# Performance work log

Hardware: AMD Instinct MI355X
Metric: run time of the kernel (lower is better)

The kernel has to match this reference:

```python
import jax, jax.numpy as jnp
import numpy as np

LN_EPS = 1e-5

def _layer_norm(x):
    mu = jnp.mean(x, axis=-1, keepdims=True)
    var = jnp.var(x, axis=-1, keepdims=True)
    return (x - mu) / jnp.sqrt(var + LN_EPS)


def setup_inputs() -> dict:
    key = jax.random.key(0)
    ks = jax.random.split(key, 3)
    B, C, H, W = 8, 384, 48, 48
    x = jax.random.normal(ks[0], (B, C, H, W), dtype=jnp.float32)
    # torch Linear default init ~ U(-1/sqrt(fan_in), 1/sqrt(fan_in)); scaled normal is fine for a reference
    W1 = jax.random.normal(ks[1], (3 * C, C), dtype=jnp.float32) / np.sqrt(C)
    b1 = jnp.zeros((3 * C,), dtype=jnp.float32)
    W2 = jax.random.normal(ks[2], (C, C), dtype=jnp.float32) / np.sqrt(C)
    b2 = jnp.zeros((C,), dtype=jnp.float32)
    return {"x": x, "W1": W1, "b1": b1, "W2": W2, "b2": b2}


def reference(x, W1, b1, W2, b2):
    num_heads = 6
    B, C, H, W = x.shape
    N = H * W
    d = C // num_heads
    # [B,C,H,W] -> [B,N,C]
    t = x.reshape(B, C, N).transpose(0, 2, 1)
    t_norm = _layer_norm(t)
    qkv = t_norm @ W1.T + b1                      # [B,N,3C]
    q, k, v = jnp.split(qkv, 3, axis=-1)
    q = q.reshape(B, N, num_heads, d).transpose(0, 2, 1, 3)  # [B,h,N,d]
    k = k.reshape(B, N, num_heads, d).transpose(0, 2, 1, 3)
    v = v.reshape(B, N, num_heads, d).transpose(0, 2, 1, 3)
    att = jnp.einsum('bhnd,bhmd->bhnm', q, k) / jnp.sqrt(jnp.float32(d))
    att = jax.nn.softmax(att, axis=-1)            # dropout_prob = 0.0 -> identity
    o = jnp.einsum('bhnm,bhmd->bhnd', att, v)     # [B,h,N,d]
    o = o.transpose(0, 2, 1, 3).reshape(B, N, C)
    o = o @ W2.T + b2
    out = (o + t_norm).transpose(0, 2, 1).reshape(B, C, H, W)
    return out
```

## Files before the change

### kernel.cpp

```cpp
#include <hip/hip_runtime.h>
#include <cstdint>

#define DEVI __device__ __forceinline__

typedef unsigned short u16;
typedef __attribute__((ext_vector_type(4))) u16 u16x4;
typedef __attribute__((ext_vector_type(2))) unsigned int u32x2;
typedef __attribute__((ext_vector_type(2))) float f32x2;
typedef __attribute__((ext_vector_type(4))) float f32x4;
typedef __attribute__((ext_vector_type(8))) float f32x8;
typedef __attribute__((ext_vector_type(16))) float f32x16;
typedef __attribute__((ext_vector_type(8))) __bf16 bf16x8;

constexpr int kB = 8, kC = 384, kN = 2304, kNH = 6, kD = 64;
constexpr int kM = kB * kN;
constexpr int k3C = 3 * kC;
constexpr int kNT = kN / 64;
constexpr int kKS = kC / 32;

DEVI float bf2f(u16 u) {
  union { unsigned int u; float f; } v; v.u = ((unsigned int)u) << 16; return v.f;
}
DEVI u16 f2bf(float f) {
  union { float f; unsigned int u; } v; v.f = f;
  return (u16)((v.u + 0x7fffu + ((v.u >> 16) & 1u)) >> 16);
}
DEVI void gload16(const void* g, void* l) {
  __builtin_amdgcn_global_load_lds(
      (__attribute__((address_space(1))) void*)const_cast<void*>(g),
      (__attribute__((address_space(3))) void*)l, 16, 0, 0);
}
DEVI bf16x8 ldg8(const u16* p) { return *reinterpret_cast<const bf16x8*>(p); }

DEVI float fexp2(float x) {
#if __has_builtin(__builtin_amdgcn_exp2f)
  return __builtin_amdgcn_exp2f(x);
#else
  return exp2f(x);
#endif
}

DEVI unsigned cvtpk(float lo, float hi) {
  unsigned r;
  asm("v_cvt_pk_bf16_f32 %0, %1, %2" : "=v"(r) : "v"(lo), "v"(hi));
  return r;
}
DEVI void plswap(unsigned& a, unsigned& b) {
#if __has_builtin(__builtin_amdgcn_permlane32_swap)
  auto rr = __builtin_amdgcn_permlane32_swap(a, b, false, false);
  a = rr[0]; b = rr[1];
#else
  unsigned ax = __shfl_xor(a, 32, 64), bx = __shfl_xor(b, 32, 64);
  int hi = (threadIdx.x & 63) >> 5;
  unsigned r0 = hi ? bx : a;
  unsigned r1 = hi ? b : ax;
  a = r0; b = r1;
#endif
}

DEVI bf16x8 ldsw(const u16* base, int row, int cb) {
  return *reinterpret_cast<const bf16x8*>(
      (const char*)base + row * 128 + (cb ^ ((row & 7) << 4)));
}

__global__ __launch_bounds__(256) void ln_kernel(const float* __restrict__ x,
                                                 u16* __restrict__ tn) {
  const int b = blockIdx.x & 7;
  const int n0 = (blockIdx.x >> 3) * 64;
  const int t = threadIdx.x;
  const int tni = t & 63, tc = t >> 6;
  const float* xb = x + (size_t)b * kC * kN;

  float sum = 0.f, ssq = 0.f;
  for (int c = tc; c < kC; c += 4) {
    float v = xb[(size_t)c * kN + n0 + tni];
    sum += v; ssq += v * v;
  }
  __shared__ float red[8][64];
  red[tc][tni] = sum; red[tc + 4][tni] = ssq;
  __syncthreads();
  __shared__ float s_mu[64], s_rs[64];
  if (t < 64) {
    float s = red[0][t] + red[1][t] + red[2][t] + red[3][t];
    float q = red[4][t] + red[5][t] + red[6][t] + red[7][t];
    float mu = s * (1.f / kC);
    float var = q * (1.f / kC) - mu * mu;
    s_mu[t] = mu; s_rs[t] = rsqrtf(var + 1e-5f);
  }
  __syncthreads();
  __shared__ float tile[64][65];
  for (int c0 = 0; c0 < kC; c0 += 64) {
#pragma unroll
    for (int kk = 0; kk < 16; ++kk) {
      int cl = tc * 16 + kk;
      tile[tni][cl] = xb[(size_t)(c0 + cl) * kN + n0 + tni];
    }
    __syncthreads();
#pragma unroll
    for (int kk = 0; kk < 16; ++kk) {
      int nl = tc * 16 + kk;
      float v = (tile[nl][tni] - s_mu[nl]) * s_rs[nl];
      tn[((size_t)b * kN + n0 + nl) * kC + c0 + tni] = f2bf(v);
    }
    __syncthreads();
  }
}

__global__ __launch_bounds__(256) void cast_w(const float* __restrict__ W1, const float* __restrict__ W2,
                                              u16* __restrict__ w1b, u16* __restrict__ w2b) {
  int i = blockIdx.x * 256 + threadIdx.x;
  if (i < k3C * kC) w1b[i] = f2bf(W1[i]);
  if (i < kC * kC)  w2b[i] = f2bf(W2[i]);
}

DEVI int swzg(int r, int sl) { return (sl ^ ((r >> 1) & 3)) * 8; }

#define GSTAGE(dstLds, gbase, kt)                                        \
  {                                                                      \
    _Pragma("unroll")                                                    \
    for (int c = 0; c < 2; ++c) {                                        \
      int i = c * 256 + t;                                               \
      int r = i >> 2, sl = i & 3;                                        \
      gload16((gbase) + (size_t)r * kC + (kt) + swzg(r, sl),             \
              (dstLds) + (c * 256 + (t & 192)) * 8);                     \
    }                                                                    \
  }

DEVI void gemm_core(const u16* __restrict__ A, const u16* __restrict__ Bm,
                    f32x4 acc[4][4], u16* lA, u16* lB) {
  const int t = threadIdx.x;
  const int lane = t & 63;
  const int w = t >> 6, wr = w >> 1, wc = w & 1;
  const int lr = lane & 15, lg = lane >> 4;

  GSTAGE(lA, A, 0)
  GSTAGE(lB, Bm, 0)

  int cur = 0;
#pragma unroll 3
  for (int s = 0; s < kKS; ++s) {
    const u16* cA = lA + cur * 4096;
    const u16* cB = lB + cur * 4096;
    const int nxt = (cur == 2) ? 0 : cur + 1;
    if (s + 1 < kKS) {
      GSTAGE(lA + nxt * 4096, A, (s + 1) * 32)
      GSTAGE(lB + nxt * 4096, Bm, (s + 1) * 32)
      asm volatile("s_waitcnt vmcnt(4)" ::: "memory");
    } else {
      asm volatile("s_waitcnt vmcnt(0)" ::: "memory");
    }
    __builtin_amdgcn_s_barrier();
    __builtin_amdgcn_sched_barrier(0);

    bf16x8 af[4], bfr[4];
#pragma unroll
    for (int f = 0; f < 4; ++f) {
      int row = wr * 64 + f * 16 + lr;
      af[f] = ldg8(&cA[row * 32 + swzg(row, lg)]);
    }
#pragma unroll
    for (int f = 0; f < 4; ++f) {
      int row = wc * 64 + f * 16 + lr;
      bfr[f] = ldg8(&cB[row * 32 + swzg(row, lg)]);
    }
    __builtin_amdgcn_s_setprio(1);
#pragma unroll
    for (int fm = 0; fm < 4; ++fm)
#pragma unroll
      for (int fn = 0; fn < 4; ++fn)
        acc[fm][fn] = __builtin_amdgcn_mfma_f32_16x16x32_bf16(af[fm], bfr[fn], acc[fm][fn], 0, 0, 0);
    __builtin_amdgcn_s_setprio(0);
    cur = nxt;
  }
}

__global__ __launch_bounds__(256) void qkv_kernel(const u16* __restrict__ tn, const u16* __restrict__ w1b,
                                                  const float* __restrict__ b1,
                                                  u16* __restrict__ q, u16* __restrict__ kbuf,
                                                  u16* __restrict__ vTout) {
  __shared__ u16 shmem[6 * 4096];
  const int wg = blockIdx.x;
  const int xcd = wg & 7, idx = wg >> 3;
  const int m0 = (xcd * 18 + idx / 9) * 128;
  const int o0 = (idx % 9) * 128;
  f32x4 acc[4][4] = {};
  gemm_core(tn + (size_t)m0 * kC, w1b + (size_t)o0 * kC, acc, shmem, shmem + 3 * 4096);

  const int t = threadIdx.x, lane = t & 63, w = t >> 6;
  const int wr = w >> 1, wc = w & 1, lr = lane & 15, lg = lane >> 4;
  const float kQScale = 0.125f * 1.44269504088896f;
  const int bb = m0 / kN;
  const int nb0 = m0 % kN;
  const int ot = o0 >> 7;

  if (ot >= 6) {
#pragma unroll
    for (int fn = 0; fn < 4; ++fn) {
      int ol = o0 - 2 * kC + wc * 64 + fn * 16 + lr;
      float bias = b1[2 * kC + ol];
      int h = ol >> 6, dd = ol & 63;
#pragma unroll
      for (int fm = 0; fm < 4; ++fm) {
        int n4 = nb0 + wr * 64 + fm * 16 + lg * 4;
        u16x4 pk;
#pragma unroll
        for (int r = 0; r < 4; ++r) pk[r] = f2bf(acc[fm][fn][r] + bias);
        *reinterpret_cast<u16x4*>(&vTout[(((size_t)bb * kNH + h) * kD + dd) * kN + n4]) = pk;
      }
    }
  } else {
    __syncthreads();
    const float scale = (ot < 3) ? kQScale : 1.0f;
#pragma unroll
    for (int fn = 0; fn < 4; ++fn) {
      int col = wc * 64 + fn * 16 + lr;
      float bias = b1[o0 + col];
#pragma unroll
      for (int fm = 0; fm < 4; ++fm)
#pragma unroll
        for (int r = 0; r < 4; ++r) {
          int row = wr * 64 + fm * 16 + lg * 4 + r;
          shmem[row * 132 + col] = f2bf((acc[fm][fn][r] + bias) * scale);
        }
    }
    __syncthreads();
    u16* outp = (ot < 3) ? q : kbuf;
    const int h0 = (o0 - (ot < 3 ? 0 : kC)) >> 6;
#pragma unroll
    for (int it = 0; it < 8; ++it) {
      int ci = it * 256 + t;
      int row = ci >> 4, ck = ci & 15;
      int c = ck * 8;
      int h = h0 + (c >> 6), dd = c & 63;
      *reinterpret_cast<bf16x8*>(&outp[(((size_t)bb * kNH + h) * kN + nb0 + row) * kD + dd]) =
          *reinterpret_cast<const bf16x8*>(&shmem[row * 132 + c]);
    }
  }
}

#define PV_STEP(SV, OFF, KS)                                                          \
  {                                                                                   \
    unsigned a0 = cvtpk(SV[OFF + 0], SV[OFF + 1]);                                    \
    unsigned a1 = cvtpk(SV[OFF + 2], SV[OFF + 3]);                                    \
    unsigned a2 = cvtpk(SV[OFF + 4], SV[OFF + 5]);                                    \
    unsigned a3 = cvtpk(SV[OFF + 6], SV[OFF + 7]);                                    \
    plswap(a0, a2); plswap(a1, a3);                                                   \
    union { unsigned wds[4]; bf16x8 v; } pu;                                          \
    pu.wds[0] = a0; pu.wds[1] = a1; pu.wds[2] = a2; pu.wds[3] = a3;                   \
    bf16x8 vf0 = ldsw(vL, ql, (KS) * 32 + hi * 16);                                   \
    bf16x8 vf1 = ldsw(vL, 32 + ql, (KS) * 32 + hi * 16);                              \
    o0 = __builtin_amdgcn_mfma_f32_32x32x16_bf16(vf0, pu.v, o0, 0, 0, 0);             \
    o1 = __builtin_amdgcn_mfma_f32_32x32x16_bf16(vf1, pu.v, o1, 0, 0, 0);             \
    o2 = __builtin_amdgcn_mfma_f32_32x32x16_bf16(onesf, pu.v, o2, 0, 0, 0);           \
  }

#define STAGE(dstLds, gbase, gstride)                                                 \
  {                                                                                   \
    int r_ = t >> 3;                                                                  \
    int cb_ = ((t & 7) * 16) ^ ((r_ & 7) << 4);                                       \
    gload16((gbase) + (size_t)r_ * (gstride) + cb_,                                   \
            (dstLds) + (t & 448) * 8);                                                \
  }

__global__ __launch_bounds__(512) void attn_kernel(const u16* __restrict__ qg, const u16* __restrict__ kg,
                                                   const u16* __restrict__ vT, u16* __restrict__ obuf) {
  const int wg = blockIdx.x;
  const int xcd = wg & 7, idx = wg >> 3;
  const int bh = xcd * 6 + idx / 9;
  const int qt = idx % 9;
  const int b = bh / kNH, h = bh % kNH;
  const int t = threadIdx.x, lane = t & 63, w = t >> 6;
  const int q0w = qt * 256 + w * 32;
  const int ql = lane & 31;
  const int hi = lane >> 5;
  const u16* qb  = qg + (size_t)bh * kN * kD;
  const char* kbB = (const char*)(kg + (size_t)bh * kN * kD);
  const char* vbT = (const char*)(vT + (size_t)bh * kD * kN);

  __shared__ u16 kLds[3 * 4096];
  __shared__ u16 vLds[3 * 4096];

  bf16x8 qf[4];
#pragma unroll
  for (int ds = 0; ds < 4; ++ds)
    qf[ds] = ldg8(&qb[(size_t)(q0w + ql) * kD + ds * 16 + hi * 8]);

  bf16x8 onesf;
#pragma unroll
  for (int j = 0; j < 8; ++j) onesf[j] = (__bf16)1.0f;

  f32x16 o0 = {}, o1 = {}, o2 = {};

  STAGE(kLds, kbB, 128)
  STAGE(vLds, vbT, kN * 2)

  int cur = 0;
  for (int ti = 0; ti < kNT; ++ti) {
    const u16* kL = kLds + cur * 4096;
    const u16* vL = vLds + cur * 4096;
    const int nxt = (cur == 2) ? 0 : cur + 1;
    if (ti + 1 < kNT) {
      const char* kNext = kbB + (size_t)(ti + 1) * 64 * 128;
      const char* vNext = vbT + (size_t)(ti + 1) * 128;
      STAGE(kLds + nxt * 4096, kNext, 128)
      STAGE(vLds + nxt * 4096, vNext, kN * 2)
      asm volatile("s_waitcnt vmcnt(2)" ::: "memory");
    } else {
      asm volatile("s_waitcnt vmcnt(0)" ::: "memory");
    }
    __builtin_amdgcn_s_barrier();
    __builtin_amdgcn_sched_barrier(0);

    f32x16 s0 = {}, s1 = {};
#pragma unroll
    for (int ds = 0; ds < 4; ++ds) {
      bf16x8 kf0 = ldsw(kL, ql, ds * 32 + hi * 16);
      bf16x8 kf1 = ldsw(kL, 32 + ql, ds * 32 + hi * 16);
      s0 = __builtin_amdgcn_mfma_f32_32x32x16_bf16(kf0, qf[ds], s0, 0, 0, 0);
      s1 = __builtin_amdgcn_mfma_f32_32x32x16_bf16(kf1, qf[ds], s1, 0, 0, 0);
    }

#pragma unroll
    for (int r = 0; r < 16; ++r) {
      s0[r] = fexp2(s0[r]);
      s1[r] = fexp2(s1[r]);
    }

    PV_STEP(s0, 0, 0)
    PV_STEP(s0, 8, 1)
    PV_STEP(s1, 0, 2)
    PV_STEP(s1, 8, 3)

    cur = nxt;
  }

  const float inv = 1.f / o2[0];
  {
    const size_t row = ((size_t)b * kN + q0w + ql) * kC + h * 64;
#pragma unroll
    for (int g = 0; g < 4; ++g) {
      u32x2 pk;
      pk.x = cvtpk(o0[g * 4 + 0] * inv, o0[g * 4 + 1] * inv);
      pk.y = cvtpk(o0[g * 4 + 2] * inv, o0[g * 4 + 3] * inv);
      *reinterpret_cast<u32x2*>(&obuf[row + g * 8 + 4 * hi]) = pk;
    }
#pragma unroll
    for (int g = 0; g < 4; ++g) {
      u32x2 pk;
      pk.x = cvtpk(o1[g * 4 + 0] * inv, o1[g * 4 + 1] * inv);
      pk.y = cvtpk(o1[g * 4 + 2] * inv, o1[g * 4 + 3] * inv);
      *reinterpret_cast<u32x2*>(&obuf[row + 32 + g * 8 + 4 * hi]) = pk;
    }
  }
}

__global__ __launch_bounds__(256) void proj_kernel(const u16* __restrict__ obuf, const u16* __restrict__ w2b,
                                                   const float* __restrict__ b2, const u16* __restrict__ tn,
                                                   float* __restrict__ out) {
  __shared__ u16 lAs[3 * 4096], lBs[3 * 4096];
  const int wg = blockIdx.x;
  const int xcd = wg & 7, idx = wg >> 3;
  const int bn = xcd * 18 + idx / 3;
  const int b = bn / 18;
  const int n0 = (bn % 18) * 128;
  const int c0 = (idx % 3) * 128;
  f32x4 acc[4][4] = {};
  gemm_core(w2b + (size_t)c0 * kC, obuf + ((size_t)b * kN + n0) * kC, acc, lAs, lBs);

  const int t = threadIdx.x, lane = t & 63, w = t >> 6;
  const int wr = w >> 1, wc = w & 1, lr = lane & 15, lg = lane >> 4;
#pragma unroll
  for (int fm = 0; fm < 4; ++fm)
#pragma unroll
    for (int fn = 0; fn < 4; ++fn) {
      int n = n0 + wc * 64 + fn * 16 + lr;
#pragma unroll
      for (int r = 0; r < 4; ++r) {
        int c = c0 + wr * 64 + fm * 16 + lg * 4 + r;
        float val = acc[fm][fn][r] + b2[c] + bf2f(tn[((size_t)b * kN + n) * kC + c]);
        out[((size_t)b * kC + c) * kN + n] = val;
      }
    }
}

extern "C" void kernel_launch(void* const* d_in, const int* in_sizes, int n_in,
                              void* d_out, int out_size, void* d_ws, size_t ws_size,
                              hipStream_t stream) {
  const float* x  = (const float*)d_in[0];
  const float* W1 = (const float*)d_in[1];
  const float* b1 = (const float*)d_in[2];
  const float* W2 = (const float*)d_in[3];
  const float* b2 = (const float*)d_in[4];
  float* out = (float*)d_out;

  const size_t nBNC = (size_t)kM * kC;
  u16* tn  = (u16*)d_ws;
  u16* qb  = tn  + nBNC;
  u16* kb  = qb  + nBNC;
  u16* vb  = kb  + nBNC;
  u16* vT  = vb  + nBNC;
  u16* w1b = vT  + nBNC;
  u16* w2b = w1b + (size_t)k3C * kC;
  u16* obuf = vb;

  ln_kernel<<<dim3(kB * (kN / 64)), dim3(256), 0, stream>>>(x, tn);
  cast_w<<<dim3((k3C * kC + 255) / 256), dim3(256), 0, stream>>>(W1, W2, w1b, w2b);
  qkv_kernel<<<dim3(kM / 128 * (k3C / 128)), dim3(256), 0, stream>>>(tn, w1b, b1, qb, kb, vT);
  attn_kernel<<<dim3((kN / 256) * kB * kNH), dim3(512), 0, stream>>>(qb, kb, vT, obuf);
  proj_kernel<<<dim3((kN / 128) * (kC / 128) * kB), dim3(256), 0, stream>>>(obuf, w2b, b2, tn, out);
}
```

Before: 168.7 us.

## Fuse weight cast into LN kernel, widen QKV GEMM tile, deepen attention prefetch

New measurement: 165.5 us. No clear change (-1.9%).

```diff
diff --git a/kernel.cpp b/kernel.cpp
--- a/kernel.cpp
+++ b/kernel.cpp
@@ -17,6 +17,8 @@
 constexpr int k3C = 3 * kC;
 constexpr int kNT = kN / 64;
 constexpr int kKS = kC / 32;
+constexpr int kW1E = k3C * kC;
+constexpr int kW2E = kC * kC;
 
 DEVI float bf2f(u16 u) {
   union { unsigned int u; float f; } v; v.u = ((unsigned int)u) << 16; return v.f;
@@ -63,8 +65,31 @@
       (const char*)base + row * 128 + (cb ^ ((row & 7) << 4)));
 }
 
-__global__ __launch_bounds__(256) void ln_kernel(const float* __restrict__ x,
-                                                 u16* __restrict__ tn) {
+__global__ __launch_bounds__(256) void ln_cast_kernel(const float* __restrict__ x,
+                                                      u16* __restrict__ tn,
+                                                      const float* __restrict__ W1,
+                                                      const float* __restrict__ W2,
+                                                      u16* __restrict__ w1b,
+                                                      u16* __restrict__ w2b) {
+  if (blockIdx.x >= 288) {
+    const int gid = (blockIdx.x - 288) * 256 + threadIdx.x;
+    const int i4 = gid * 4;
+    if (i4 < kW1E) {
+      f32x4 v = *reinterpret_cast<const f32x4*>(&W1[i4]);
+      u16x4 o;
+#pragma unroll
+      for (int r = 0; r < 4; ++r) o[r] = f2bf(v[r]);
+      *reinterpret_cast<u16x4*>(&w1b[i4]) = o;
+    } else if (i4 < kW1E + kW2E) {
+      const int j = i4 - kW1E;
+      f32x4 v = *reinterpret_cast<const f32x4*>(&W2[j]);
+      u16x4 o;
+#pragma unroll
+      for (int r = 0; r < 4; ++r) o[r] = f2bf(v[r]);
+      *reinterpret_cast<u16x4*>(&w2b[j]) = o;
+    }
+    return;
+  }
   const int b = blockIdx.x & 7;
   const int n0 = (blockIdx.x >> 3) * 64;
   const int t = threadIdx.x;
@@ -104,13 +129,6 @@
     }
     __syncthreads();
   }
-}
-
-__global__ __launch_bounds__(256) void cast_w(const float* __restrict__ W1, const float* __restrict__ W2,
-                                              u16* __restrict__ w1b, u16* __restrict__ w2b) {
-  int i = blockIdx.x * 256 + threadIdx.x;
-  if (i < k3C * kC) w1b[i] = f2bf(W1[i]);
-  if (i < kC * kC)  w2b[i] = f2bf(W2[i]);
 }
 
 DEVI int swzg(int r, int sl) { return (sl ^ ((r >> 1) & 3)) * 8; }
@@ -174,23 +192,88 @@
   }
 }
 
-__global__ __launch_bounds__(256) void qkv_kernel(const u16* __restrict__ tn, const u16* __restrict__ w1b,
+#define GSTAGE2A(dstLds, gbase, kt)                                      \
+  {                                                                      \
+    _Pragma("unroll")                                                    \
+    for (int c = 0; c < 2; ++c) {                                        \
+      int i = c * 512 + t;                                               \
+      int r = i >> 2, sl = i & 3;                                        \
+      gload16((gbase) + (size_t)r * kC + (kt) + swzg(r, sl),             \
+              (dstLds) + (c * 512 + (t & 448)) * 8);                     \
+    }                                                                    \
+  }
+#define GSTAGE2B(dstLds, gbase, kt)                                      \
+  {                                                                      \
+    int r = t >> 2, sl = t & 3;                                          \
+    gload16((gbase) + (size_t)r * kC + (kt) + swzg(r, sl),               \
+            (dstLds) + (t & 448) * 8);                                   \
+  }
+
+DEVI void gemm_core256(const u16* __restrict__ A, const u16* __restrict__ Bm,
+                       f32x4 acc[4][4], u16* lA, u16* lB) {
+  const int t = threadIdx.x;
+  const int lane = t & 63;
+  const int w = t >> 6, wr = w >> 1, wc = w & 1;
+  const int lr = lane & 15, lg = lane >> 4;
+
+  GSTAGE2A(lA, A, 0)
+  GSTAGE2B(lB, Bm, 0)
+
+  int cur = 0;
+#pragma unroll 3
+  for (int s = 0; s < kKS; ++s) {
+    const u16* cA = lA + cur * 8192;
+    const u16* cB = lB + cur * 4096;
+    const int nxt = (cur == 2) ? 0 : cur + 1;
+    if (s + 1 < kKS) {
+      GSTAGE2A(lA + nxt * 8192, A, (s + 1) * 32)
+      GSTAGE2B(lB + nxt * 4096, Bm, (s + 1) * 32)
+      asm volatile("s_waitcnt vmcnt(3)" ::: "memory");
+    } else {
+      asm volatile("s_waitcnt vmcnt(0)" ::: "memory");
+    }
+    __builtin_amdgcn_s_barrier();
+    __builtin_amdgcn_sched_barrier(0);
+
+    bf16x8 af[4], bfr[4];
+#pragma unroll
+    for (int f = 0; f < 4; ++f) {
+      int row = wr * 64 + f * 16 + lr;
+      af[f] = ldg8(&cA[row * 32 + swzg(row, lg)]);
+    }
+#pragma unroll
+    for (int f = 0; f < 4; ++f) {
+      int row = wc * 64 + f * 16 + lr;
+      bfr[f] = ldg8(&cB[row * 32 + swzg(row, lg)]);
+    }
+    __builtin_amdgcn_s_setprio(1);
+#pragma unroll
+    for (int fm = 0; fm < 4; ++fm)
+#pragma unroll
+      for (int fn = 0; fn < 4; ++fn)
+        acc[fm][fn] = __builtin_amdgcn_mfma_f32_16x16x32_bf16(af[fm], bfr[fn], acc[fm][fn], 0, 0, 0);
+    __builtin_amdgcn_s_setprio(0);
+    cur = nxt;
+  }
+}
+
+__global__ __launch_bounds__(512) void qkv_kernel(const u16* __restrict__ tn, const u16* __restrict__ w1b,
                                                   const float* __restrict__ b1,
                                                   u16* __restrict__ q, u16* __restrict__ kbuf,
                                                   u16* __restrict__ vTout) {
-  __shared__ u16 shmem[6 * 4096];
+  __shared__ u16 shmem[36864];
   const int wg = blockIdx.x;
   const int xcd = wg & 7, idx = wg >> 3;
-  const int m0 = (xcd * 18 + idx / 9) * 128;
+  const int m0 = (xcd * 9 + idx / 9) * 256;
   const int o0 = (idx % 9) * 128;
   f32x4 acc[4][4] = {};
-  gemm_core(tn + (size_t)m0 * kC, w1b + (size_t)o0 * kC, acc, shmem, shmem + 3 * 4096);
+  gemm_core256(tn + (size_t)m0 * kC, w1b + (size_t)o0 * kC, acc, shmem, shmem + 3 * 8192);
 
   const int t = threadIdx.x, lane = t & 63, w = t >> 6;
   const int wr = w >> 1, wc = w & 1, lr = lane & 15, lg = lane >> 4;
   const float kQScale = 0.125f * 1.44269504088896f;
-  const int bb = m0 / kN;
-  const int nb0 = m0 % kN;
+  const int bb = xcd;
+  const int nb0 = (idx / 9) * 256;
   const int ot = o0 >> 7;
 
   if (ot >= 6) {
@@ -228,7 +311,7 @@
     const int h0 = (o0 - (ot < 3 ? 0 : kC)) >> 6;
 #pragma unroll
     for (int it = 0; it < 8; ++it) {
-      int ci = it * 256 + t;
+      int ci = it * 512 + t;
       int row = ci >> 4, ck = ci & 15;
       int c = ck * 8;
       int h = h0 + (c >> 6), dd = c & 63;
@@ -277,8 +360,8 @@
   const char* kbB = (const char*)(kg + (size_t)bh * kN * kD);
   const char* vbT = (const char*)(vT + (size_t)bh * kD * kN);
 
-  __shared__ u16 kLds[3 * 4096];
-  __shared__ u16 vLds[3 * 4096];
+  __shared__ u16 kLds[4 * 4096];
+  __shared__ u16 vLds[4 * 4096];
 
   bf16x8 qf[4];
 #pragma unroll
@@ -293,17 +376,21 @@
 
   STAGE(kLds, kbB, 128)
   STAGE(vLds, vbT, kN * 2)
+  STAGE(kLds + 4096, kbB + (size_t)64 * 128, 128)
+  STAGE(vLds + 4096, vbT + 128, kN * 2)
 
   int cur = 0;
   for (int ti = 0; ti < kNT; ++ti) {
     const u16* kL = kLds + cur * 4096;
     const u16* vL = vLds + cur * 4096;
-    const int nxt = (cur == 2) ? 0 : cur + 1;
-    if (ti + 1 < kNT) {
-      const char* kNext = kbB + (size_t)(ti + 1) * 64 * 128;
-      const char* vNext = vbT + (size_t)(ti + 1) * 128;
-      STAGE(kLds + nxt * 4096, kNext, 128)
-      STAGE(vLds + nxt * 4096, vNext, kN * 2)
+    if (ti + 2 < kNT) {
+      const int stg = (cur + 2) & 3;
+      const char* kNext = kbB + (size_t)(ti + 2) * 64 * 128;
+      const char* vNext = vbT + (size_t)(ti + 2) * 128;
+      STAGE(kLds + stg * 4096, kNext, 128)
+      STAGE(vLds + stg * 4096, vNext, kN * 2)
+      asm volatile("s_waitcnt vmcnt(4)" ::: "memory");
+    } else if (ti + 1 < kNT) {
       asm volatile("s_waitcnt vmcnt(2)" ::: "memory");
     } else {
       asm volatile("s_waitcnt vmcnt(0)" ::: "memory");
@@ -331,7 +418,7 @@
     PV_STEP(s1, 0, 2)
     PV_STEP(s1, 8, 3)
 
-    cur = nxt;
+    cur = (cur + 1) & 3;
   }
 
   const float inv = 1.f / o2[0];
@@ -403,9 +490,8 @@
   u16* w2b = w1b + (size_t)k3C * kC;
   u16* obuf = vb;
 
-  ln_kernel<<<dim3(kB * (kN / 64)), dim3(256), 0, stream>>>(x, tn);
-  cast_w<<<dim3((k3C * kC + 255) / 256), dim3(256), 0, stream>>>(W1, W2, w1b, w2b);
-  qkv_kernel<<<dim3(kM / 128 * (k3C / 128)), dim3(256), 0, stream>>>(tn, w1b, b1, qb, kb, vT);
+  ln_cast_kernel<<<dim3(288 + 576), dim3(256), 0, stream>>>(x, tn, W1, W2, w1b, w2b);
+  qkv_kernel<<<dim3(8 * 81), dim3(512), 0, stream>>>(tn, w1b, b1, qb, kb, vT);
   attn_kernel<<<dim3((kN / 256) * kB * kNH), dim3(512), 0, stream>>>(qb, kb, vT, obuf);
   proj_kernel<<<dim3((kN / 128) * (kC / 128) * kB), dim3(256), 0, stream>>>(obuf, w2b, b2, tn, out);
 }
```
